# Optimization experiments

Measured on AMD Instinct MI355X. Metric: run time of the kernel, lower is better.

Reference implementation:

```python
import jax, jax.numpy as jnp
import numpy as np

N_MOLS = 2048
DEPTH = 4

def _graph_conv(fatoms, fbonds, agraph, bgraph, Wi, Wh, Wo, bo):
    # fbonds: [n_bonds, 88] -> nei_input_h: [n_bonds, H]
    nei_input_h = fbonds @ Wi.T
    msg = jax.nn.relu(nei_input_h)
    for _ in range(DEPTH - 1):
        # gather neighbor bond messages [n_bonds, max_nei, H], sum over neighbors
        nei = msg[bgraph].sum(axis=1)
        msg = jax.nn.relu(nei_input_h + nei @ Wh.T)
    # aggregate bond messages into atoms: [n_atoms, max_nei, H] -> [n_atoms, H]
    atom_nei = msg[agraph].sum(axis=1)
    atom_in = jnp.concatenate([fatoms, atom_nei], axis=1)  # [n_atoms, 82+H]
    return jax.nn.relu(atom_in @ Wo.T + bo)

def _mol_embed(atom_h, mol_idx):
    return jax.ops.segment_sum(atom_h, mol_idx, num_segments=N_MOLS)

def setup_inputs() -> dict:
    key = jax.random.key(0)
    ks = jax.random.split(key, 24)
    n_atoms, n_bonds, max_nei, H = 100000, 200000, 10, 256
    d = {}
    d['fatoms_src'] = jax.random.normal(ks[0], (n_atoms, 82), jnp.float32)
    d['fbonds_src'] = jax.random.normal(ks[1], (n_bonds, 88), jnp.float32)
    d['agraph_src'] = jax.random.randint(ks[2], (n_atoms, max_nei), 0, n_bonds, jnp.int32)
    d['bgraph_src'] = jax.random.randint(ks[3], (n_bonds, max_nei), 0, n_bonds, jnp.int32)
    d['mol_idx_src'] = jnp.sort(jax.random.randint(ks[4], (n_atoms,), 0, N_MOLS, jnp.int32))
    d['fatoms_tgt'] = jax.random.normal(ks[5], (n_atoms, 82), jnp.float32)
    d['fbonds_tgt'] = jax.random.normal(ks[6], (n_bonds, 88), jnp.float32)
    d['agraph_tgt'] = jax.random.randint(ks[7], (n_atoms, max_nei), 0, n_bonds, jnp.int32)
    d['bgraph_tgt'] = jax.random.randint(ks[8], (n_bonds, max_nei), 0, n_bonds, jnp.int32)
    d['mol_idx_tgt'] = jnp.sort(jax.random.randint(ks[9], (n_atoms,), 0, N_MOLS, jnp.int32))
    s = 0.05
    d['Wi_s'] = jax.random.normal(ks[10], (H, 88), jnp.float32) * s
    d['Wh_s'] = jax.random.normal(ks[11], (H, H), jnp.float32) * s
    d['Wo_s'] = jax.random.normal(ks[12], (H, 82 + H), jnp.float32) * s
    d['bo_s'] = jax.random.normal(ks[13], (H,), jnp.float32) * s
    d['Wi_t'] = jax.random.normal(ks[14], (H, 88), jnp.float32) * s
    d['Wh_t'] = jax.random.normal(ks[15], (H, H), jnp.float32) * s
    d['Wo_t'] = jax.random.normal(ks[16], (H, 82 + H), jnp.float32) * s
    d['bo_t'] = jax.random.normal(ks[17], (H,), jnp.float32) * s
    d['Wrh'] = jax.random.normal(ks[18], (H, H), jnp.float32) * s
    d['brh'] = jax.random.normal(ks[19], (H,), jnp.float32) * s
    d['Wro'] = jax.random.normal(ks[20], (1, H), jnp.float32) * s
    d['bro'] = jax.random.normal(ks[21], (1,), jnp.float32) * s
    return d

def reference(fatoms_src, fbonds_src, agraph_src, bgraph_src, mol_idx_src,
              fatoms_tgt, fbonds_tgt, agraph_tgt, bgraph_tgt, mol_idx_tgt,
              Wi_s, Wh_s, Wo_s, bo_s, Wi_t, Wh_t, Wo_t, bo_t,
              Wrh, brh, Wro, bro):
    src_atom_h = _graph_conv(fatoms_src, fbonds_src, agraph_src, bgraph_src, Wi_s, Wh_s, Wo_s, bo_s)
    src_mol_h = _mol_embed(src_atom_h, mol_idx_src)
    tgt_atom_h = _graph_conv(fatoms_tgt, fbonds_tgt, agraph_tgt, bgraph_tgt, Wi_t, Wh_t, Wo_t, bo_t)
    tgt_mol_h = _mol_embed(tgt_atom_h, mol_idx_tgt)
    rxn_h = jax.nn.relu((tgt_mol_h - src_mol_h) @ Wrh.T + brh)
    return rxn_h @ Wro.T + bro  # [N_MOLS, 1]
```

## Files before the change

kernel.cpp:

```cpp
#include <hip/hip_runtime.h>

typedef _Float16 f16;
using f16x8 = __attribute__((ext_vector_type(8))) _Float16;
using f32x4 = __attribute__((ext_vector_type(4))) float;

#define H 256
#define NM 2048

template<int N> struct Int { static constexpr int v = N; };

__device__ __forceinline__ void gload_lds16(const f16* g, f16* lds)
{
    __builtin_amdgcn_global_load_lds(
        (const __attribute__((address_space(1))) void*)g,
        (__attribute__((address_space(3))) void*)lds, 16, 0, 0);
}

__global__ __launch_bounds__(256, 3) void gemm_fused(
    const float* __restrict__ A1, int lda1, int K1r,
    const f16*  __restrict__ W1,
    const f16*  __restrict__ src2, const int* __restrict__ idx2,
    const f16*  __restrict__ W2,
    const float* __restrict__ bias, f16* __restrict__ C, int M)
{
    __shared__ f16 Bs[256][64];

    const int bm   = blockIdx.x * 64;
    const int tid  = threadIdx.x;
    const int wave = tid >> 6, lane = tid & 63;
    const int lrow = lane & 15;
    const int kg   = lane >> 4;
    const int swz  = lrow & 7;

    const int glr = lane >> 3;
    const int gsc = (lane & 7) ^ glr;

    const int  myrow = bm + wave * 16 + lrow;
    const bool rowok = myrow < M;

    f32x4 acc[16];
    #pragma unroll
    for (int n = 0; n < 16; ++n) acc[n] = (f32x4){0.f, 0.f, 0.f, 0.f};

    f16x8 af[8];

    auto stageB = [&](const f16* W, int ldw, int k0) {
        #pragma unroll
        for (int q = 0; q < 8; ++q)
            gload_lds16(W + (size_t)(wave * 64 + q * 8 + glr) * ldw + k0 + gsc * 8,
                        &Bs[wave * 64 + q * 8][0]);
    };

    auto windows = [&](auto NW, const f16* W, int ldw) {
        constexpr int nw = decltype(NW)::v;
        #pragma unroll
        for (int w = 0; w < nw; ++w) {
            stageB(W, ldw, w * 64);
            __syncthreads();
            #pragma unroll
            for (int ks = 0; ks < 2; ++ks) {
                const int cb = ((ks * 4 + kg) ^ swz) * 8;
                const f16x8 a = af[w * 2 + ks];
                #pragma unroll
                for (int n = 0; n < 16; ++n) {
                    f16x8 b = *(const f16x8*)&Bs[n * 16 + lrow][cb];
                    acc[n] = __builtin_amdgcn_mfma_f32_16x16x32_f16(a, b, acc[n], 0, 0, 0);
                }
            }
            __syncthreads();
        }
    };

    if (A1 != nullptr) {
        #pragma unroll
        for (int t = 0; t < 4; ++t) {
            const int k0 = (4 * t + kg) * 8;
            const float* sp = A1 + (size_t)myrow * lda1 + k0;
            f16 tmp[8];
            #pragma unroll
            for (int i = 0; i < 8; i += 2) {
                float x = 0.f, y = 0.f;
                if (rowok) {
                    if (k0 + i + 1 < K1r) { float2 v = *(const float2*)(sp + i); x = v.x; y = v.y; }
                    else if (k0 + i < K1r) { x = sp[i]; }
                }
                tmp[i] = (f16)x; tmp[i + 1] = (f16)y;
            }
            af[t] = *(const f16x8*)tmp;
        }
        windows(Int<2>{}, W1, 128);
    }

    if (src2 != nullptr) {
        if (idx2 != nullptr) {
            int ip[10];
            if (rowok) {
                const int* p = idx2 + (size_t)myrow * 10;
                #pragma unroll
                for (int j = 0; j < 10; ++j) ip[j] = p[j];
            } else {
                #pragma unroll
                for (int j = 0; j < 10; ++j) ip[j] = 0;
            }
            const f16* base = src2 + kg * 8;
            #pragma unroll
            for (int t = 0; t < 8; ++t) {
                f16x8 vA = *(const f16x8*)(base + (size_t)ip[0] * H + t * 32);
                f16x8 vB = *(const f16x8*)(base + (size_t)ip[1] * H + t * 32);
                #pragma unroll
                for (int j = 2; j < 10; j += 2) {
                    f16x8 u0 = *(const f16x8*)(base + (size_t)ip[j]     * H + t * 32);
                    f16x8 u1 = *(const f16x8*)(base + (size_t)ip[j + 1] * H + t * 32);
                    vA = vA + u0;
                    vB = vB + u1;
                }
                f16x8 s = vA + vB;
                if (!rowok) {
                    #pragma unroll
                    for (int e = 0; e < 8; ++e) s[e] = (f16)0.f;
                }
                af[t] = s;
            }
        } else {
            #pragma unroll
            for (int t = 0; t < 8; ++t) {
                if (rowok)
                    af[t] = *(const f16x8*)(src2 + (size_t)myrow * H + kg * 8 + t * 32);
                else {
                    #pragma unroll
                    for (int e = 0; e < 8; ++e) af[t][e] = (f16)0.f;
                }
            }
        }
        windows(Int<4>{}, W2, 256);
    }

    #pragma unroll
    for (int n = 0; n < 16; ++n) {
        const int gc = n * 16 + lrow;
        const float bv = bias ? bias[gc] : 0.f;
        #pragma unroll
        for (int r = 0; r < 4; ++r) {
            const int gr = bm + wave * 16 + kg * 4 + r;
            if (gr < M) C[(size_t)gr * H + gc] = (f16)fmaxf(acc[n][r] + bv, 0.f);
        }
    }
}

__global__ __launch_bounds__(256) void convert_w(
    const float* __restrict__ src, int lds_, int koff, int kvalid,
    f16* __restrict__ dst, int Kd)
{
    int n = blockIdx.x;
    for (int k = threadIdx.x; k < Kd; k += 256) {
        float v = (k < kvalid) ? src[(size_t)n * lds_ + koff + k] : 0.f;
        dst[(size_t)n * Kd + k] = (f16)v;
    }
}

__global__ __launch_bounds__(256) void segsum(
    const f16* __restrict__ atom_h, const int* __restrict__ mol_idx,
    float* __restrict__ mol_h, int n_atoms)
{
    int m = blockIdx.x;
    int lo = 0, hi = n_atoms;
    while (lo < hi) { int mid = (lo + hi) >> 1; if (mol_idx[mid] < m) lo = mid + 1; else hi = mid; }
    int start = lo;
    hi = n_atoms;
    while (lo < hi) { int mid = (lo + hi) >> 1; if (mol_idx[mid] < m + 1) lo = mid + 1; else hi = mid; }
    int end = lo;
    int c = threadIdx.x;
    float s = 0.f;
    for (int a = start; a < end; ++a) s += (float)atom_h[(size_t)a * H + c];
    mol_h[(size_t)m * H + c] = s;
}

__global__ __launch_bounds__(256) void diff_kernel(
    const float* __restrict__ a, const float* __restrict__ b,
    f16* __restrict__ c, int n)
{
    int i = blockIdx.x * 256 + threadIdx.x;
    if (i < n) c[i] = (f16)(a[i] - b[i]);
}

__global__ __launch_bounds__(256) void final_dot(
    const f16* __restrict__ rxn, const float* __restrict__ Wro,
    const float* __restrict__ bro, float* __restrict__ out)
{
    int m = blockIdx.x;
    int t = threadIdx.x;
    float v = (float)rxn[(size_t)m * H + t] * Wro[t];
    #pragma unroll
    for (int off = 32; off; off >>= 1) v += __shfl_down(v, off, 64);
    __shared__ float red[4];
    if ((t & 63) == 0) red[t >> 6] = v;
    __syncthreads();
    if (t == 0) out[m] = red[0] + red[1] + red[2] + red[3] + bro[0];
}

static void run_graph(const float* fatoms, const float* fbonds, const int* agraph,
                      const int* bgraph, const int* mol_idx,
                      const f16* Wi16, const f16* Wh16, const f16* Wo1, const f16* Wo2,
                      const float* bo,
                      f16* bufA, f16* bufB, float* molh,
                      int n_atoms, int n_bonds, hipStream_t stream)
{
    dim3 gb((n_bonds + 63) / 64);
    dim3 ga((n_atoms + 63) / 64);

    gemm_fused<<<gb, 256, 0, stream>>>(fbonds, 88, 88, Wi16,
                                       (const f16*)nullptr, (const int*)nullptr,
                                       (const f16*)nullptr,
                                       (const float*)nullptr, bufA, n_bonds);
    f16* cur = bufA; f16* nxt = bufB;
    for (int it = 0; it < 3; ++it) {
        gemm_fused<<<gb, 256, 0, stream>>>(fbonds, 88, 88, Wi16,
                                           cur, bgraph, Wh16,
                                           (const float*)nullptr, nxt, n_bonds);
        f16* t = cur; cur = nxt; nxt = t;
    }
    gemm_fused<<<ga, 256, 0, stream>>>(fatoms, 82, 82, Wo1,
                                       cur, agraph, Wo2,
                                       bo, nxt, n_atoms);
    segsum<<<NM, 256, 0, stream>>>(nxt, mol_idx, molh, n_atoms);
}

extern "C" void kernel_launch(void* const* d_in, const int* in_sizes, int n_in,
                              void* d_out, int out_size, void* d_ws, size_t ws_size,
                              hipStream_t stream)
{
    const float* fatoms_src = (const float*)d_in[0];
    const float* fbonds_src = (const float*)d_in[1];
    const int*   agraph_src = (const int*)d_in[2];
    const int*   bgraph_src = (const int*)d_in[3];
    const int*   mol_idx_src= (const int*)d_in[4];
    const float* fatoms_tgt = (const float*)d_in[5];
    const float* fbonds_tgt = (const float*)d_in[6];
    const int*   agraph_tgt = (const int*)d_in[7];
    const int*   bgraph_tgt = (const int*)d_in[8];
    const int*   mol_idx_tgt= (const int*)d_in[9];
    const float* Wi_s = (const float*)d_in[10];
    const float* Wh_s = (const float*)d_in[11];
    const float* Wo_s = (const float*)d_in[12];
    const float* bo_s = (const float*)d_in[13];
    const float* Wi_t = (const float*)d_in[14];
    const float* Wh_t = (const float*)d_in[15];
    const float* Wo_t = (const float*)d_in[16];
    const float* bo_t = (const float*)d_in[17];
    const float* Wrh  = (const float*)d_in[18];
    const float* brh  = (const float*)d_in[19];
    const float* Wro  = (const float*)d_in[20];
    const float* bro  = (const float*)d_in[21];

    const int n_atoms = in_sizes[0] / 82;
    const int n_bonds = in_sizes[1] / 88;

    char* ws = (char*)d_ws;
    size_t off = 0;
    auto alloc = [&](size_t bytes) { size_t o = off; off = (off + bytes + 255) & ~(size_t)255; return o; };
    f16*   bufA = (f16*)(ws + alloc((size_t)n_bonds * H * 2));
    f16*   bufB = (f16*)(ws + alloc((size_t)n_bonds * H * 2));
    float* molS = (float*)(ws + alloc((size_t)NM * H * 4));
    float* molT = (float*)(ws + alloc((size_t)NM * H * 4));
    f16*   dbuf = (f16*)(ws + alloc((size_t)NM * H * 2));
    f16*   rxn  = (f16*)(ws + alloc((size_t)NM * H * 2));
    f16* Wi16_s = (f16*)(ws + alloc(256 * 128 * 2));
    f16* Wh16_s = (f16*)(ws + alloc(256 * 256 * 2));
    f16* Wo1_s  = (f16*)(ws + alloc(256 * 128 * 2));
    f16* Wo2_s  = (f16*)(ws + alloc(256 * 256 * 2));
    f16* Wi16_t = (f16*)(ws + alloc(256 * 128 * 2));
    f16* Wh16_t = (f16*)(ws + alloc(256 * 256 * 2));
    f16* Wo1_t  = (f16*)(ws + alloc(256 * 128 * 2));
    f16* Wo2_t  = (f16*)(ws + alloc(256 * 256 * 2));
    f16* Wrh16  = (f16*)(ws + alloc(256 * 256 * 2));

    convert_w<<<256, 256, 0, stream>>>(Wi_s,  88,  0,  88, Wi16_s, 128);
    convert_w<<<256, 256, 0, stream>>>(Wh_s, 256,  0, 256, Wh16_s, 256);
    convert_w<<<256, 256, 0, stream>>>(Wo_s, 338,  0,  82, Wo1_s, 128);
    convert_w<<<256, 256, 0, stream>>>(Wo_s, 338, 82, 256, Wo2_s, 256);
    convert_w<<<256, 256, 0, stream>>>(Wi_t,  88,  0,  88, Wi16_t, 128);
    convert_w<<<256, 256, 0, stream>>>(Wh_t, 256,  0, 256, Wh16_t, 256);
    convert_w<<<256, 256, 0, stream>>>(Wo_t, 338,  0,  82, Wo1_t, 128);
    convert_w<<<256, 256, 0, stream>>>(Wo_t, 338, 82, 256, Wo2_t, 256);
    convert_w<<<256, 256, 0, stream>>>(Wrh, 256,  0, 256, Wrh16, 256);

    run_graph(fatoms_src, fbonds_src, agraph_src, bgraph_src, mol_idx_src,
              Wi16_s, Wh16_s, Wo1_s, Wo2_s, bo_s,
              bufA, bufB, molS, n_atoms, n_bonds, stream);
    run_graph(fatoms_tgt, fbonds_tgt, agraph_tgt, bgraph_tgt, mol_idx_tgt,
              Wi16_t, Wh16_t, Wo1_t, Wo2_t, bo_t,
              bufA, bufB, molT, n_atoms, n_bonds, stream);

    diff_kernel<<<(NM * H + 255) / 256, 256, 0, stream>>>(molT, molS, dbuf, NM * H);
    gemm_fused<<<NM / 64, 256, 0, stream>>>((const float*)nullptr, 0, 0, (const f16*)nullptr,
                                            dbuf, (const int*)nullptr, Wrh16,
                                            brh, rxn, NM);
    final_dot<<<NM, 256, 0, stream>>>(rxn, Wro, bro, (float*)d_out);
}
```

Baseline: 2.667 ms.

## Software-pipeline neighbor gather with MFMA windows and raise occupancy to 4

Replaces the up-front gather of all eight A fragments with a per-window gather that is double-buffered, so the gather for window w+1 is issued while the MFMAs for window w run. Cutting the live A fragments from eight to four lowers register pressure, and launch bounds are raised from 3 to 4 blocks per CU for more latency hiding. The risks are register spills under the tighter bound, and gather loads now sitting between barriers, which can serialize with the LDS staging.

```diff
diff --git a/kernel.cpp b/kernel.cpp
--- a/kernel.cpp
+++ b/kernel.cpp
@@ -7,8 +7,6 @@
 #define H 256
 #define NM 2048
 
-template<int N> struct Int { static constexpr int v = N; };
-
 __device__ __forceinline__ void gload_lds16(const f16* g, f16* lds)
 {
     __builtin_amdgcn_global_load_lds(
@@ -16,7 +14,7 @@
         (__attribute__((address_space(3))) void*)lds, 16, 0, 0);
 }
 
-__global__ __launch_bounds__(256, 3) void gemm_fused(
+__global__ __launch_bounds__(256, 4) void gemm_fused(
     const float* __restrict__ A1, int lda1, int K1r,
     const f16*  __restrict__ W1,
     const f16*  __restrict__ src2, const int* __restrict__ idx2,
@@ -42,8 +40,6 @@
     #pragma unroll
     for (int n = 0; n < 16; ++n) acc[n] = (f32x4){0.f, 0.f, 0.f, 0.f};
 
-    f16x8 af[8];
-
     auto stageB = [&](const f16* W, int ldw, int k0) {
         #pragma unroll
         for (int q = 0; q < 8; ++q)
@@ -51,49 +47,49 @@
                         &Bs[wave * 64 + q * 8][0]);
     };
 
-    auto windows = [&](auto NW, const f16* W, int ldw) {
-        constexpr int nw = decltype(NW)::v;
-        #pragma unroll
-        for (int w = 0; w < nw; ++w) {
-            stageB(W, ldw, w * 64);
+    auto mfma_win = [&](f16x8 a0, f16x8 a1) {
+        #pragma unroll
+        for (int ks = 0; ks < 2; ++ks) {
+            const int cb = ((ks * 4 + kg) ^ swz) * 8;
+            const f16x8 av = ks ? a1 : a0;
+            #pragma unroll
+            for (int n = 0; n < 16; ++n) {
+                f16x8 b = *(const f16x8*)&Bs[n * 16 + lrow][cb];
+                acc[n] = __builtin_amdgcn_mfma_f32_16x16x32_f16(av, b, acc[n], 0, 0, 0);
+            }
+        }
+    };
+
+    if (A1 != nullptr) {
+        #pragma unroll
+        for (int w = 0; w < 2; ++w) {
+            f16x8 a[2];
+            #pragma unroll
+            for (int c = 0; c < 2; ++c) {
+                const int k0 = (w * 8 + c * 4 + kg) * 8;
+                const float* sp = A1 + (size_t)myrow * lda1 + k0;
+                f16 tmp[8];
+                #pragma unroll
+                for (int i = 0; i < 8; i += 2) {
+                    float x = 0.f, y = 0.f;
+                    if (rowok) {
+                        if (k0 + i + 1 < K1r) { float2 v = *(const float2*)(sp + i); x = v.x; y = v.y; }
+                        else if (k0 + i < K1r) { x = sp[i]; }
+                    }
+                    tmp[i] = (f16)x; tmp[i + 1] = (f16)y;
+                }
+                a[c] = *(const f16x8*)tmp;
+            }
+            stageB(W1, 128, w * 64);
             __syncthreads();
-            #pragma unroll
-            for (int ks = 0; ks < 2; ++ks) {
-                const int cb = ((ks * 4 + kg) ^ swz) * 8;
-                const f16x8 a = af[w * 2 + ks];
-                #pragma unroll
-                for (int n = 0; n < 16; ++n) {
-                    f16x8 b = *(const f16x8*)&Bs[n * 16 + lrow][cb];
-                    acc[n] = __builtin_amdgcn_mfma_f32_16x16x32_f16(a, b, acc[n], 0, 0, 0);
-                }
-            }
+            mfma_win(a[0], a[1]);
             __syncthreads();
         }
-    };
-
-    if (A1 != nullptr) {
-        #pragma unroll
-        for (int t = 0; t < 4; ++t) {
-            const int k0 = (4 * t + kg) * 8;
-            const float* sp = A1 + (size_t)myrow * lda1 + k0;
-            f16 tmp[8];
-            #pragma unroll
-            for (int i = 0; i < 8; i += 2) {
-                float x = 0.f, y = 0.f;
-                if (rowok) {
-                    if (k0 + i + 1 < K1r) { float2 v = *(const float2*)(sp + i); x = v.x; y = v.y; }
-                    else if (k0 + i < K1r) { x = sp[i]; }
-                }
-                tmp[i] = (f16)x; tmp[i + 1] = (f16)y;
-            }
-            af[t] = *(const f16x8*)tmp;
-        }
-        windows(Int<2>{}, W1, 128);
     }
 
     if (src2 != nullptr) {
+        int ip[10];
         if (idx2 != nullptr) {
-            int ip[10];
             if (rowok) {
                 const int* p = idx2 + (size_t)myrow * 10;
                 #pragma unroll
@@ -102,37 +98,48 @@
                 #pragma unroll
                 for (int j = 0; j < 10; ++j) ip[j] = 0;
             }
-            const f16* base = src2 + kg * 8;
+        }
+
+        f16x8 a[2][2];
+        auto gather_win = [&](int w, f16x8* dst) {
             #pragma unroll
-            for (int t = 0; t < 8; ++t) {
-                f16x8 vA = *(const f16x8*)(base + (size_t)ip[0] * H + t * 32);
-                f16x8 vB = *(const f16x8*)(base + (size_t)ip[1] * H + t * 32);
-                #pragma unroll
-                for (int j = 2; j < 10; j += 2) {
-                    f16x8 u0 = *(const f16x8*)(base + (size_t)ip[j]     * H + t * 32);
-                    f16x8 u1 = *(const f16x8*)(base + (size_t)ip[j + 1] * H + t * 32);
-                    vA = vA + u0;
-                    vB = vB + u1;
-                }
-                f16x8 s = vA + vB;
-                if (!rowok) {
+            for (int c = 0; c < 2; ++c) {
+                const int chunk = w * 8 + c * 4 + kg;
+                if (idx2 != nullptr) {
+                    const f16* base = src2 + (size_t)chunk * 8;
+                    f16x8 vA = *(const f16x8*)(base + (size_t)ip[0] * H);
+                    f16x8 vB = *(const f16x8*)(base + (size_t)ip[1] * H);
                     #pragma unroll
-                    for (int e = 0; e < 8; ++e) s[e] = (f16)0.f;
-                }
-                af[t] = s;
-            }
-        } else {
-            #pragma unroll
-            for (int t = 0; t < 8; ++t) {
-                if (rowok)
-                    af[t] = *(const f16x8*)(src2 + (size_t)myrow * H + kg * 8 + t * 32);
-                else {
-                    #pragma unroll
-                    for (int e = 0; e < 8; ++e) af[t][e] = (f16)0.f;
+                    for (int j = 2; j < 10; j += 2) {
+                        vA = vA + *(const f16x8*)(base + (size_t)ip[j]     * H);
+                        vB = vB + *(const f16x8*)(base + (size_t)ip[j + 1] * H);
+                    }
+                    f16x8 s = vA + vB;
+                    if (!rowok) {
+                        #pragma unroll
+                        for (int e = 0; e < 8; ++e) s[e] = (f16)0.f;
+                    }
+                    dst[c] = s;
+                } else {
+                    if (rowok)
+                        dst[c] = *(const f16x8*)(src2 + (size_t)myrow * H + chunk * 8);
+                    else {
+                        #pragma unroll
+                        for (int e = 0; e < 8; ++e) dst[c][e] = (f16)0.f;
+                    }
                 }
             }
-        }
-        windows(Int<4>{}, W2, 256);
+        };
+
+        gather_win(0, a[0]);
+        #pragma unroll
+        for (int w = 0; w < 4; ++w) {
+            stageB(W2, H, w * 64);
+            __syncthreads();
+            if (w < 3) gather_win(w + 1, a[(w + 1) & 1]);
+            mfma_win(a[w & 1][0], a[w & 1][1]);
+            __syncthreads();
+        }
     }
 
     #pragma unroll
```

Result: slower. 3.004 ms, median of 5 (+12.6%).
